# Performance work log

Measured on AMD Instinct MI355X. Metric: run time of the kernel, lower is better.

The kernel has to match this reference:

```python
import jax, jax.numpy as jnp
import numpy as np

BN_EPS = 1e-5
K = 3  # kernel size


def conv2d(x, w, b, pad):
    y = jax.lax.conv_general_dilated(
        x, w, window_strides=(1, 1), padding=[(pad, pad), (pad, pad)],
        dimension_numbers=('NCHW', 'OIHW', 'NCHW'))
    return y + b[None, :, None, None]


def setup_inputs() -> dict:
    key = jax.random.key(0)
    ks = jax.random.split(key, 4)
    B, C, H, W, O = 8, 256, 64, 64, 256
    x = jax.random.normal(ks[0], (B, C, H, W), dtype=jnp.float32)
    # offset/mask conv: 3*dg*k*k = 27 out channels; small init -> small offsets
    w_off = jax.random.normal(ks[1], (27, C, K, K), dtype=jnp.float32) * 0.01
    b_off = jnp.zeros((27,), dtype=jnp.float32)
    # main deformable conv weight/bias
    w = jax.random.normal(ks[2], (O, C, K, K), dtype=jnp.float32) * 0.05
    b = jnp.zeros((O,), dtype=jnp.float32)
    # BatchNorm (inference) params / running stats
    gamma = jnp.ones((O,), dtype=jnp.float32)
    beta = jnp.zeros((O,), dtype=jnp.float32)
    run_mean = jnp.zeros((O,), dtype=jnp.float32)
    run_var = jnp.ones((O,), dtype=jnp.float32)
    return {"x": x, "w_off": w_off, "b_off": b_off, "w": w, "b": b,
            "gamma": gamma, "beta": beta, "run_mean": run_mean, "run_var": run_var}


def _dcn_bn_relu(x, w_off, b_off, w, b, gamma, beta, run_mean, run_var):
    B, C, H, W = x.shape
    KK = K * K
    # offset + modulation mask (DCNv2): channels [0:9]=dy, [9:18]=dx, [18:27]=mask
    om = conv2d(x, w_off, b_off, pad=1)            # [B, 27, H, W]
    dy, dx = om[:, :KK], om[:, KK:2 * KK]          # [B, 9, H, W]
    mod = jax.nn.sigmoid(om[:, 2 * KK:])           # [B, 9, H, W]

    ky, kx = jnp.meshgrid(jnp.arange(K), jnp.arange(K), indexing='ij')
    # base sampling grid: out pixel + dilation*(k - center), padding=1
    base_y = jnp.arange(H, dtype=jnp.float32)[None, :, None] - 1.0 + ky.reshape(KK, 1, 1)
    base_x = jnp.arange(W, dtype=jnp.float32)[None, None, :] - 1.0 + kx.reshape(KK, 1, 1)
    py = base_y[None] + dy                          # [B, 9, H, W]
    px = base_x[None] + dx

    y0 = jnp.floor(py); x0 = jnp.floor(px)
    fy = py - y0; fx = px - x0
    y0 = y0.astype(jnp.int32); x0 = x0.astype(jnp.int32)

    x_flat = x.reshape(B, C, H * W)
    gather = jax.vmap(lambda xf, idx: xf[:, idx])   # ([C,HW],[9,H,W]) -> [C,9,H,W]

    def corner(yi, xi, wgt):
        valid = (yi >= 0) & (yi < H) & (xi >= 0) & (xi < W)
        idx = jnp.clip(yi, 0, H - 1) * W + jnp.clip(xi, 0, W - 1)
        val = gather(x_flat, idx)                   # [B, C, 9, H, W]
        return val * (wgt * valid.astype(wgt.dtype))[:, None]

    sampled = (corner(y0,     x0,     (1 - fy) * (1 - fx))
               + corner(y0,     x0 + 1, (1 - fy) * fx)
               + corner(y0 + 1, x0,     fy * (1 - fx))
               + corner(y0 + 1, x0 + 1, fy * fx))    # [B, C, 9, H, W]
    sampled = sampled * mod[:, None]                 # modulation

    O = w.shape[0]
    out = jnp.einsum('bckhw,ock->bohw', sampled, w.reshape(O, C, KK))
    out = out + b[None, :, None, None]

    # BatchNorm2d (inference) + ReLU
    inv = gamma / jnp.sqrt(run_var + BN_EPS)
    out = out * inv[None, :, None, None] + (beta - run_mean * inv)[None, :, None, None]
    return jax.nn.relu(out)


def reference(x, w_off, b_off, w, b, gamma, beta, run_mean, run_var):
    return _dcn_bn_relu(x, w_off, b_off, w, b, gamma, beta, run_mean, run_var)
```

## Files before the change

kernel.cpp:

```cpp
#include <hip/hip_runtime.h>
#include <math.h>

#define B_   8
#define C_   256
#define H_   64
#define W_   64
#define O_   256
#define KK_  9
#define CK_  2304
#define HW_  4096
#define BN_EPS 1e-5f

typedef __bf16 bf16x8 __attribute__((ext_vector_type(8)));
typedef float  f32x4  __attribute__((ext_vector_type(4)));

static __device__ __forceinline__ unsigned short f2bf(float f) {
    unsigned int u = __float_as_uint(f);
    unsigned int r = (u + 0x7fffu + ((u >> 16) & 1u)) >> 16;
    return (unsigned short)r;
}
static __device__ __forceinline__ unsigned int packbf2(float lo, float hi) {
    unsigned int ul = __float_as_uint(lo) + 0x8000u;
    unsigned int uh = __float_as_uint(hi) + 0x8000u;
    return __builtin_amdgcn_perm(uh, ul, 0x07060302u);
}
static __device__ __forceinline__ float bflo(unsigned int u) {
    return __uint_as_float(u << 16);
}
static __device__ __forceinline__ float bfhi(unsigned int u) {
    return __uint_as_float(u & 0xffff0000u);
}

__global__ __launch_bounds__(256) void prep_kernel(
    const float* __restrict__ x, const float* __restrict__ w,
    const float* __restrict__ w_off,
    unsigned short* __restrict__ xT, unsigned short* __restrict__ wKf,
    unsigned short* __restrict__ wof)
{
    __shared__ float tile[64][65];
    __shared__ float wbuf[4608];

    const int blk = blockIdx.x;
    const int tid = threadIdx.x, lane = tid & 63, tg = tid >> 6;

    if (blk < 512) {
        const int b = blk & 7, h = blk >> 3;
        const int hwb = h * W_;
#pragma unroll
        for (int ct = 0; ct < 4; ++ct) {
            const int c0 = ct * 64;
#pragma unroll
            for (int r = 0; r < 16; ++r) {
                int c_l = tg + r * 4;
                tile[c_l][lane] = x[((size_t)(b * C_ + c0 + c_l)) * HW_ + hwb + lane];
            }
            __syncthreads();
#pragma unroll
            for (int it = 0; it < 4; ++it) {
                const int hw_l = tg * 16 + it * 4 + (lane >> 4);
                const int c_l4 = (lane & 15) * 4;
                float v0 = tile[c_l4 + 0][hw_l];
                float v1 = tile[c_l4 + 1][hw_l];
                float v2 = tile[c_l4 + 2][hw_l];
                float v3 = tile[c_l4 + 3][hw_l];
                uint2 pk;
                pk.x = packbf2(v0, v1);
                pk.y = packbf2(v2, v3);
                *(uint2*)&xT[((size_t)(b * HW_ + hwb + hw_l)) * C_ + c0 + c_l4] = pk;
            }
            __syncthreads();
        }
    } else if (blk < 640) {
        const int t2 = blk - 512;
        const int NT = t2 >> 3, cb = t2 & 7;
#pragma unroll
        for (int i = 0; i < 18; ++i) {
            int j = i * 256 + tid;
            int o_l = j / 288, rest = j - o_l * 288;
            wbuf[o_l * 288 + rest] = w[(size_t)(NT * 16 + o_l) * CK_ + cb * 288 + rest];
        }
        __syncthreads();
#pragma unroll
        for (int i = 0; i < 18; ++i) {
            int d = i * 256 + tid;
            int tap = d >> 9, r5 = d & 511;
            int ln = r5 >> 3, e = r5 & 7;
            int n16 = ln & 15, q = ln >> 4;
            float val = wbuf[n16 * 288 + (q * 8 + e) * 9 + tap];
            wKf[((size_t)(NT * 72 + tap * 8 + cb) * 64 + ln) * 8 + e] = f2bf(val);
        }
    } else {
        const int t2 = blk - 640;
        const int NT = t2 >> 3, cb = t2 & 7;
#pragma unroll
        for (int i = 0; i < 18; ++i) {
            int j = i * 256 + tid;
            int o_l = j / 288, rest = j - o_l * 288;
            int o = NT * 16 + o_l;
            wbuf[o_l * 288 + rest] =
                (o < 27) ? w_off[(size_t)o * CK_ + cb * 288 + rest] : 0.f;
        }
        __syncthreads();
#pragma unroll
        for (int i = 0; i < 18; ++i) {
            int d = i * 256 + tid;
            int tap = d >> 9, r5 = d & 511;
            int ln = r5 >> 3, e = r5 & 7;
            int n16 = ln & 15, q = ln >> 4;
            float val = wbuf[n16 * 288 + (q * 8 + e) * 9 + tap];
            wof[((size_t)(NT * 72 + tap * 8 + cb) * 64 + ln) * 8 + e] = f2bf(val);
        }
    }
}

__global__ __launch_bounds__(512, 4) void dcn_fused_kernel(
    const unsigned short* __restrict__ xT, const unsigned short* __restrict__ wKf,
    const unsigned short* __restrict__ wof, const float* __restrict__ b_off,
    const float* __restrict__ bias, const float* __restrict__ gamma,
    const float* __restrict__ beta, const float* __restrict__ rmean,
    const float* __restrict__ rvar, float* __restrict__ out)
{
    __shared__ __align__(16) unsigned char smem[74528];
    unsigned short* rowbuf = (unsigned short*)smem;
    float4*         wgtv   = (float4*)smem;
    int4*           idxv   = (int4*)(smem + 9216);
    typedef float OmbT[27][64];
    OmbT& omb = *(OmbT*)(smem + 34848);
    typedef unsigned short AbufT[8][4][64][8];
    AbufT& Abuf = *(AbufT*)(smem + 41760);

    const int blk = blockIdx.x;
    const int b = blk & 7, h = blk >> 3;
    const int tid = threadIdx.x, lane = tid & 63, wv = tid >> 6;
    const int m16 = lane & 15, q = lane >> 4;

    if (tid < 33) {
        *(uint4*)&rowbuf[tid * 8] = make_uint4(0u, 0u, 0u, 0u);
    } else if (tid >= 256 && tid < 289) {
        *(uint4*)&rowbuf[65 * 264 + (tid - 256) * 8] = make_uint4(0u, 0u, 0u, 0u);
    }

    const int mi_a = wv & 3, nj_a = wv >> 2;
    f32x4 oacc = {0.f, 0.f, 0.f, 0.f};
    const uint4* wof4 = (const uint4*)wof;

    for (int r = 0; r < 3; ++r) {
        const int hh = h - 1 + r;
        const bool vr = (hh >= 0) && (hh < H_);
        __syncthreads();
        if (vr) {
            const uint4* src = (const uint4*)&xT[((size_t)(b * HW_ + hh * W_)) * C_];
#pragma unroll
            for (int i = 0; i < 4; ++i) {
                const int idx8 = i * 512 + tid;
                uint4 v = src[idx8];
                const int px = idx8 >> 5, c8 = (idx8 & 31) * 8;
                *(uint4*)&rowbuf[(px + 1) * 264 + c8] = v;
            }
        }
        __syncthreads();
        if (vr) {
#pragma unroll
            for (int s = 0; s < 3; ++s) {
                const unsigned short* arow = &rowbuf[(mi_a * 16 + m16 + s) * 264 + q * 8];
#pragma unroll
                for (int cc = 0; cc < 8; ++cc) {
                    bf16x8 a = *(const bf16x8*)&arow[cc * 32];
                    uint4 braw = wof4[(size_t)(nj_a * 72 + (r * 3 + s) * 8 + cc) * 64 + lane];
                    oacc = __builtin_amdgcn_mfma_f32_16x16x32_bf16(
                        a, __builtin_bit_cast(bf16x8, braw), oacc, 0, 0, 0);
                }
            }
        }
    }
    {
        const int t = nj_a * 16 + m16;
        if (t < 27) {
            const float bo = b_off[t];
            float s0 = oacc[0] + bo, s1 = oacc[1] + bo,
                  s2 = oacc[2] + bo, s3 = oacc[3] + bo;
            if (t >= 18) {
                s0 = 1.f / (1.f + expf(-s0));
                s1 = 1.f / (1.f + expf(-s1));
                s2 = 1.f / (1.f + expf(-s2));
                s3 = 1.f / (1.f + expf(-s3));
            }
            float4 rr; rr.x = s0; rr.y = s1; rr.z = s2; rr.w = s3;
            *(float4*)&omb[t][mi_a * 16 + q * 4] = rr;
        }
    }
    __syncthreads();

    for (int i = tid; i < 576; i += 512) {
        int p = i / 9, t = i - p * 9;
        float dy = omb[t][p];
        float dx = omb[t + 9][p];
        float md = omb[t + 18][p];
        float py = (float)(h - 1 + t / 3) + dy;
        float px = (float)(p - 1 + t % 3) + dx;
        float y0f = floorf(py), x0f = floorf(px);
        int   y0 = (int)y0f,    x0 = (int)x0f;
        float fy = py - y0f,    fx = px - x0f;
        int y0c = min(max(y0,     0), H_ - 1), y1c = min(max(y0 + 1, 0), H_ - 1);
        int x0c = min(max(x0,     0), W_ - 1), x1c = min(max(x0 + 1, 0), W_ - 1);
        float vy0 = (y0     >= 0 && y0     < H_) ? 1.f : 0.f;
        float vy1 = (y0 + 1 >= 0 && y0 + 1 < H_) ? 1.f : 0.f;
        float vx0 = (x0     >= 0 && x0     < W_) ? 1.f : 0.f;
        float vx1 = (x0 + 1 >= 0 && x0 + 1 < W_) ? 1.f : 0.f;
        wgtv[i] = make_float4((1.f - fy) * (1.f - fx) * vy0 * vx0 * md,
                              (1.f - fy) * fx         * vy0 * vx1 * md,
                              fy         * (1.f - fx) * vy1 * vx0 * md,
                              fy         * fx         * vy1 * vx1 * md);
        const int rowb = (b * HW_) * (C_ * 2);
        idxv[i] = make_int4(rowb + (y0c * W_ + x0c) * (C_ * 2),
                            rowb + (y0c * W_ + x1c) * (C_ * 2),
                            rowb + (y1c * W_ + x0c) * (C_ * 2),
                            rowb + (y1c * W_ + x1c) * (C_ * 2));
    }
    __syncthreads();

    f32x4 acc[4][2];
#pragma unroll
    for (int mi = 0; mi < 4; ++mi)
#pragma unroll
        for (int nj = 0; nj < 2; ++nj)
#pragma unroll
            for (int r = 0; r < 4; ++r) acc[mi][nj][r] = 0.f;

    const uint4* wKf4 = (const uint4*)wKf;
    const char*  xTb  = (const char*)xT;

    const int s_cc = lane >> 3;
    const int s_q2 = (lane >> 1) & 3;
    const int s_j0 = (lane & 1) * 4;
    const int s_xr = (s_q2 << 1) ^ s_cc;
    const int s_mi = wv >> 1;
    const int s_pb = (wv & 1) * 8;
    const int loff = lane * 8;

    const int r_row = lane ^ ((lane >> 4) << 1);

    for (int tap = 0; tap < 9; ++tap) {
        uint2 pk[8];
#pragma unroll
        for (int pp = 0; pp < 8; ++pp) {
            const int p = wv * 8 + pp;
            const int4   iq = idxv[p * 9 + tap];
            const float4 wq = wgtv[p * 9 + tap];
            const uint2 k0 = *(const uint2*)(xTb + iq.x + loff);
            const uint2 k1 = *(const uint2*)(xTb + iq.y + loff);
            const uint2 k2 = *(const uint2*)(xTb + iq.z + loff);
            const uint2 k3 = *(const uint2*)(xTb + iq.w + loff);
            float g0 = wq.x*bflo(k0.x) + wq.y*bflo(k1.x) + wq.z*bflo(k2.x) + wq.w*bflo(k3.x);
            float g1 = wq.x*bfhi(k0.x) + wq.y*bfhi(k1.x) + wq.z*bfhi(k2.x) + wq.w*bfhi(k3.x);
            float g2 = wq.x*bflo(k0.y) + wq.y*bflo(k1.y) + wq.z*bflo(k2.y) + wq.w*bflo(k3.y);
            float g3 = wq.x*bfhi(k0.y) + wq.y*bfhi(k1.y) + wq.z*bfhi(k2.y) + wq.w*bfhi(k3.y);
            pk[pp].x = packbf2(g0, g1);
            pk[pp].y = packbf2(g2, g3);
        }

        __syncthreads();
#pragma unroll
        for (int pp = 0; pp < 8; ++pp) {
            const int P   = s_pb + pp;
            const int row = (P ^ s_xr) | (s_q2 << 4);
            *(uint2*)&Abuf[s_cc][s_mi][row][s_j0] = pk[pp];
        }
        __syncthreads();

#pragma unroll
        for (int cc = 0; cc < 8; ++cc) {
            const int KC = tap * 8 + cc;
            const int rr = r_row ^ cc;
            uint4 braw[2];
#pragma unroll
            for (int nj = 0; nj < 2; ++nj)
                braw[nj] = wKf4[(size_t)((wv * 2 + nj) * 72 + KC) * 64 + lane];
            bf16x8 a[4];
#pragma unroll
            for (int mi = 0; mi < 4; ++mi)
                a[mi] = *(const bf16x8*)&Abuf[cc][mi][rr][0];
#pragma unroll
            for (int nj = 0; nj < 2; ++nj) {
                bf16x8 bb = __builtin_bit_cast(bf16x8, braw[nj]);
#pragma unroll
                for (int mi = 0; mi < 4; ++mi)
                    acc[mi][nj] = __builtin_amdgcn_mfma_f32_16x16x32_bf16(
                        a[mi], bb, acc[mi][nj], 0, 0, 0);
            }
        }
    }

#pragma unroll
    for (int nj = 0; nj < 2; ++nj) {
        const int o = wv * 32 + nj * 16 + (lane & 15);
        const float inv = gamma[o] * rsqrtf(rvar[o] + BN_EPS);
        const float sh  = beta[o] + (bias[o] - rmean[o]) * inv;
        float* ob = out + ((size_t)(b * O_ + o)) * HW_ + h * W_;
#pragma unroll
        for (int mi = 0; mi < 4; ++mi) {
            f32x4 v = acc[mi][nj];
            float4 r;
            r.x = fmaxf(v[0] * inv + sh, 0.f);
            r.y = fmaxf(v[1] * inv + sh, 0.f);
            r.z = fmaxf(v[2] * inv + sh, 0.f);
            r.w = fmaxf(v[3] * inv + sh, 0.f);
            *(float4*)&ob[mi * 16 + (lane >> 4) * 4] = r;
        }
    }
}

extern "C" void kernel_launch(void* const* d_in, const int* in_sizes, int n_in,
                              void* d_out, int out_size, void* d_ws, size_t ws_size,
                              hipStream_t stream) {
    const float* x     = (const float*)d_in[0];
    const float* w_off = (const float*)d_in[1];
    const float* b_off = (const float*)d_in[2];
    const float* w     = (const float*)d_in[3];
    const float* bias  = (const float*)d_in[4];
    const float* gamma = (const float*)d_in[5];
    const float* beta  = (const float*)d_in[6];
    const float* rmean = (const float*)d_in[7];
    const float* rvar  = (const float*)d_in[8];
    float* out = (float*)d_out;

    unsigned short* xT  = (unsigned short*)d_ws;
    unsigned short* wKf = xT + 8388608;
    unsigned short* wof = wKf + 589824;

    prep_kernel<<<656, 256, 0, stream>>>(x, w, w_off, xT, wKf, wof);
    dcn_fused_kernel<<<512, 512, 0, stream>>>(
        xT, wKf, wof, b_off, bias, gamma, beta, rmean, rvar, out);
}
```

Baseline: 183.1 us.

## Split transpose into finer blocks and read offset-conv inputs directly from global

The prep kernel's x transpose is split from 512 blocks each handling four channel tiles into 2048 blocks each handling one 64x64 tile, which increases parallelism and drops the per-tile syncs. In the fused kernel, the offset-conv stage no longer stages input rows in shared memory. It loads A fragments straight from the global transposed buffer, with boundary masking. This removes barriers and shrinks shared memory from about 73KB to 50KB, which may allow more resident blocks, at the cost of redundant global/L2 reads across the three horizontal taps.

Result: slower. 206.2 us (+12.6%).

```diff
diff --git a/kernel.cpp b/kernel.cpp
--- a/kernel.cpp
+++ b/kernel.cpp
@@ -43,35 +43,32 @@
     const int blk = blockIdx.x;
     const int tid = threadIdx.x, lane = tid & 63, tg = tid >> 6;
 
-    if (blk < 512) {
-        const int b = blk & 7, h = blk >> 3;
-        const int hwb = h * W_;
-#pragma unroll
-        for (int ct = 0; ct < 4; ++ct) {
-            const int c0 = ct * 64;
-#pragma unroll
-            for (int r = 0; r < 16; ++r) {
-                int c_l = tg + r * 4;
-                tile[c_l][lane] = x[((size_t)(b * C_ + c0 + c_l)) * HW_ + hwb + lane];
-            }
-            __syncthreads();
-#pragma unroll
-            for (int it = 0; it < 4; ++it) {
-                const int hw_l = tg * 16 + it * 4 + (lane >> 4);
-                const int c_l4 = (lane & 15) * 4;
-                float v0 = tile[c_l4 + 0][hw_l];
-                float v1 = tile[c_l4 + 1][hw_l];
-                float v2 = tile[c_l4 + 2][hw_l];
-                float v3 = tile[c_l4 + 3][hw_l];
-                uint2 pk;
-                pk.x = packbf2(v0, v1);
-                pk.y = packbf2(v2, v3);
-                *(uint2*)&xT[((size_t)(b * HW_ + hwb + hw_l)) * C_ + c0 + c_l4] = pk;
-            }
-            __syncthreads();
-        }
-    } else if (blk < 640) {
-        const int t2 = blk - 512;
+    if (blk < 2048) {
+        const int b   = blk & 7;
+        const int ct  = (blk >> 3) & 3;
+        const int hwt = blk >> 5;
+        const int c0  = ct * 64, hw0 = hwt * 64;
+#pragma unroll
+        for (int r = 0; r < 16; ++r) {
+            int c_l = tg + r * 4;
+            tile[c_l][lane] = x[((size_t)(b * C_ + c0 + c_l)) * HW_ + hw0 + lane];
+        }
+        __syncthreads();
+#pragma unroll
+        for (int it = 0; it < 4; ++it) {
+            const int hw_l = tg * 16 + it * 4 + (lane >> 4);
+            const int c_l4 = (lane & 15) * 4;
+            float v0 = tile[c_l4 + 0][hw_l];
+            float v1 = tile[c_l4 + 1][hw_l];
+            float v2 = tile[c_l4 + 2][hw_l];
+            float v3 = tile[c_l4 + 3][hw_l];
+            uint2 pk;
+            pk.x = packbf2(v0, v1);
+            pk.y = packbf2(v2, v3);
+            *(uint2*)&xT[((size_t)(b * HW_ + hw0 + hw_l)) * C_ + c0 + c_l4] = pk;
+        }
+    } else if (blk < 2176) {
+        const int t2 = blk - 2048;
         const int NT = t2 >> 3, cb = t2 & 7;
 #pragma unroll
         for (int i = 0; i < 18; ++i) {
@@ -90,7 +87,7 @@
             wKf[((size_t)(NT * 72 + tap * 8 + cb) * 64 + ln) * 8 + e] = f2bf(val);
         }
     } else {
-        const int t2 = blk - 640;
+        const int t2 = blk - 2176;
         const int NT = t2 >> 3, cb = t2 & 7;
 #pragma unroll
         for (int i = 0; i < 18; ++i) {
@@ -120,56 +117,42 @@
     const float* __restrict__ beta, const float* __restrict__ rmean,
     const float* __restrict__ rvar, float* __restrict__ out)
 {
-    __shared__ __align__(16) unsigned char smem[74528];
-    unsigned short* rowbuf = (unsigned short*)smem;
-    float4*         wgtv   = (float4*)smem;
-    int4*           idxv   = (int4*)(smem + 9216);
+    __shared__ __align__(16) unsigned char smem[51200];
+    float4* wgtv = (float4*)smem;
+    int4*   idxv = (int4*)(smem + 9216);
     typedef float OmbT[27][64];
-    OmbT& omb = *(OmbT*)(smem + 34848);
+    OmbT& omb = *(OmbT*)(smem + 18432);
     typedef unsigned short AbufT[8][4][64][8];
-    AbufT& Abuf = *(AbufT*)(smem + 41760);
+    AbufT& Abuf = *(AbufT*)(smem + 18432);
 
     const int blk = blockIdx.x;
     const int b = blk & 7, h = blk >> 3;
     const int tid = threadIdx.x, lane = tid & 63, wv = tid >> 6;
     const int m16 = lane & 15, q = lane >> 4;
 
-    if (tid < 33) {
-        *(uint4*)&rowbuf[tid * 8] = make_uint4(0u, 0u, 0u, 0u);
-    } else if (tid >= 256 && tid < 289) {
-        *(uint4*)&rowbuf[65 * 264 + (tid - 256) * 8] = make_uint4(0u, 0u, 0u, 0u);
-    }
-
     const int mi_a = wv & 3, nj_a = wv >> 2;
+    const int pxa  = mi_a * 16 + m16;
     f32x4 oacc = {0.f, 0.f, 0.f, 0.f};
     const uint4* wof4 = (const uint4*)wof;
 
+#pragma unroll
     for (int r = 0; r < 3; ++r) {
         const int hh = h - 1 + r;
-        const bool vr = (hh >= 0) && (hh < H_);
-        __syncthreads();
-        if (vr) {
-            const uint4* src = (const uint4*)&xT[((size_t)(b * HW_ + hh * W_)) * C_];
-#pragma unroll
-            for (int i = 0; i < 4; ++i) {
-                const int idx8 = i * 512 + tid;
-                uint4 v = src[idx8];
-                const int px = idx8 >> 5, c8 = (idx8 & 31) * 8;
-                *(uint4*)&rowbuf[(px + 1) * 264 + c8] = v;
-            }
-        }
-        __syncthreads();
-        if (vr) {
-#pragma unroll
-            for (int s = 0; s < 3; ++s) {
-                const unsigned short* arow = &rowbuf[(mi_a * 16 + m16 + s) * 264 + q * 8];
-#pragma unroll
-                for (int cc = 0; cc < 8; ++cc) {
-                    bf16x8 a = *(const bf16x8*)&arow[cc * 32];
-                    uint4 braw = wof4[(size_t)(nj_a * 72 + (r * 3 + s) * 8 + cc) * 64 + lane];
-                    oacc = __builtin_amdgcn_mfma_f32_16x16x32_bf16(
-                        a, __builtin_bit_cast(bf16x8, braw), oacc, 0, 0, 0);
-                }
+        if (hh < 0 || hh >= H_) continue;
+        const unsigned short* rowp = xT + ((size_t)(b * HW_ + hh * W_)) * C_ + q * 8;
+#pragma unroll
+        for (int s = 0; s < 3; ++s) {
+            const int ww = pxa + s - 1;
+            const bool ok = ((unsigned)ww) < (unsigned)W_;
+            const unsigned short* pbase = rowp + ww * C_;
+#pragma unroll
+            for (int cc = 0; cc < 8; ++cc) {
+                uint4 araw = ok ? *(const uint4*)(pbase + cc * 32)
+                                : make_uint4(0u, 0u, 0u, 0u);
+                uint4 braw = wof4[(size_t)(nj_a * 72 + (r * 3 + s) * 8 + cc) * 64 + lane];
+                oacc = __builtin_amdgcn_mfma_f32_16x16x32_bf16(
+                    __builtin_bit_cast(bf16x8, araw),
+                    __builtin_bit_cast(bf16x8, braw), oacc, 0, 0, 0);
             }
         }
     }
@@ -328,7 +311,7 @@
     unsigned short* wKf = xT + 8388608;
     unsigned short* wof = wKf + 589824;
 
-    prep_kernel<<<656, 256, 0, stream>>>(x, w, w_off, xT, wKf, wof);
+    prep_kernel<<<2192, 256, 0, stream>>>(x, w, w_off, xT, wKf, wof);
     dcn_fused_kernel<<<512, 512, 0, stream>>>(
         xT, wKf, wof, b_off, bias, gamma, beta, rmean, rvar, out);
 }
```
